# Kernel optimization log

Hardware: AMD Instinct MI355X
Metric: run time of the kernel (lower is better)

The kernel has to match this reference:

```python
import jax, jax.numpy as jnp
import numpy as np

LATENT_PACKET_SIZE = 16

def setup_inputs() -> dict:
    key = jax.random.key(0)
    z = jax.random.normal(key, (4096, 1, 8192), dtype=jnp.float32)
    return {"z": z}

def reference(z) -> jnp.ndarray:
    B = z.shape[0]
    D = z.shape[2]
    P = LATENT_PACKET_SIZE
    n_packets = D // P
    zp = z.reshape(B, n_packets, P)                      # (B, N, P)
    # sort packets within each sample by the first element of each packet
    inds = jnp.argsort(zp[:, :, 0], axis=1)              # (B, N) int
    z_ordered = jnp.take_along_axis(zp, inds[:, :, None], axis=1)  # batched gather
    return z_ordered.reshape(B, 1, n_packets * P)
```

## Files before the change

kernel.cpp:

```cpp
#include <hip/hip_runtime.h>


#define NPK 512
#define DIM 8192
#define RPB 4
#define NT  256

__global__ __launch_bounds__(NT, 8)
void sort_latent_kernel(const float* __restrict__ z, float* __restrict__ out) {
    __shared__ unsigned long long keys[RPB][NPK];
    __shared__ unsigned short     srcp[RPB][NPK];

    const int lane = threadIdx.x & 63;
    const int w    = threadIdx.x >> 6;
    const int row  = blockIdx.x * RPB + w;
    const float* __restrict__ rowin  = z   + (size_t)row * DIM;
    float*       __restrict__ rowout = out + (size_t)row * DIM;

    unsigned long long myk[8];
#pragma unroll
    for (int i = 0; i < 8; ++i) {
        const unsigned int p = (unsigned)(i * 64 + lane);
        const unsigned int b = __float_as_uint(rowin[p * 16]);
        const unsigned int u = b ^ (((unsigned)((int)b >> 31)) | 0x80000000u);
        myk[i] = ((unsigned long long)u << 32) | p;
        keys[w][p] = myk[i];
    }
    __syncthreads();

    unsigned int rank[8] = {0, 0, 0, 0, 0, 0, 0, 0};
    const unsigned long long* __restrict__ kk = keys[w];
    for (int j = 0; j < NPK; j += 2) {
        const unsigned long long k0 = kk[j];
        const unsigned long long k1 = kk[j + 1];
#pragma unroll
        for (int i = 0; i < 8; ++i) {
            rank[i] += (unsigned)(k0 < myk[i]);
            rank[i] += (unsigned)(k1 < myk[i]);
        }
    }
#pragma unroll
    for (int i = 0; i < 8; ++i)
        srcp[w][rank[i]] = (unsigned short)(i * 64 + lane);
    __syncthreads();

    const float4* __restrict__ in4  = (const float4*)rowin;
    float4*       __restrict__ out4 = (float4*)rowout;
#pragma unroll 8
    for (int i = 0; i < DIM / 4 / 64; ++i) {
        const int o = i * 64 + lane;
        const int s = (int)srcp[w][o >> 2];
        out4[o] = in4[(s << 2) | (o & 3)];
    }
}

extern "C" void kernel_launch(void* const* d_in, const int* in_sizes, int n_in,
                              void* d_out, int out_size, void* d_ws, size_t ws_size,
                              hipStream_t stream) {
    const float* z = (const float*)d_in[0];
    float* out = (float*)d_out;
    const int nrows = in_sizes[0] / DIM;
    sort_latent_kernel<<<nrows / RPB, NT, 0, stream>>>(z, out);
}
```

Before: 251.9 us.

## Replace O(N^2) rank counting with register bitonic sort using wave shuffles

Swaps the per-row all-pairs rank counting, which reads every key from LDS for each of 512 keys, for a bitonic sort. Each lane holds 8 consecutive keys in registers; small strides use in-register compare-exchange and larger strides use 64-bit cross-lane shuffles. This drops the keys LDS array and one barrier and cuts comparisons from about 256K to about 12K per row. The cost is many 64-bit shuffles, which need two DPP/permute ops each, and index-dependent select logic.

```diff
diff --git a/kernel.cpp b/kernel.cpp
--- a/kernel.cpp
+++ b/kernel.cpp
@@ -6,10 +6,18 @@
 #define RPB 4
 #define NT  256
 
+typedef unsigned long long u64;
+
+#define CEX(a, b, up) {                      \
+    bool sw = ((a) > (b)) == (up);           \
+    u64 t0 = sw ? (b) : (a);                 \
+    (b) = sw ? (a) : (b);                    \
+    (a) = t0;                                \
+}
+
 __global__ __launch_bounds__(NT, 8)
 void sort_latent_kernel(const float* __restrict__ z, float* __restrict__ out) {
-    __shared__ unsigned long long keys[RPB][NPK];
-    __shared__ unsigned short     srcp[RPB][NPK];
+    __shared__ unsigned short srcp[RPB][NPK];
 
     const int lane = threadIdx.x & 63;
     const int w    = threadIdx.x >> 6;
@@ -17,31 +25,46 @@
     const float* __restrict__ rowin  = z   + (size_t)row * DIM;
     float*       __restrict__ rowout = out + (size_t)row * DIM;
 
-    unsigned long long myk[8];
+    u64 v[8];
 #pragma unroll
-    for (int i = 0; i < 8; ++i) {
-        const unsigned int p = (unsigned)(i * 64 + lane);
-        const unsigned int b = __float_as_uint(rowin[p * 16]);
-        const unsigned int u = b ^ (((unsigned)((int)b >> 31)) | 0x80000000u);
-        myk[i] = ((unsigned long long)u << 32) | p;
-        keys[w][p] = myk[i];
+    for (int r = 0; r < 8; ++r) {
+        const unsigned p = (unsigned)(lane * 8 + r);
+        const unsigned b = __float_as_uint(rowin[p * 16]);
+        const unsigned u = b ^ (((unsigned)((int)b >> 31)) | 0x80000000u);
+        v[r] = ((u64)u << 32) | p;
     }
-    __syncthreads();
 
-    unsigned int rank[8] = {0, 0, 0, 0, 0, 0, 0, 0};
-    const unsigned long long* __restrict__ kk = keys[w];
-    for (int j = 0; j < NPK; j += 2) {
-        const unsigned long long k0 = kk[j];
-        const unsigned long long k1 = kk[j + 1];
+    CEX(v[0], v[1], true);  CEX(v[2], v[3], false);
+    CEX(v[4], v[5], true);  CEX(v[6], v[7], false);
+    CEX(v[0], v[2], true);  CEX(v[1], v[3], true);
+    CEX(v[4], v[6], false); CEX(v[5], v[7], false);
+    CEX(v[0], v[1], true);  CEX(v[2], v[3], true);
+    CEX(v[4], v[5], false); CEX(v[6], v[7], false);
+
+    for (int k = 8; k <= NPK; k <<= 1) {
+        const bool up = ((lane & (k >> 3)) == 0);
+        for (int j = k >> 1; j >= 8; j >>= 1) {
+            const int d = j >> 3;
+            const bool keepmin = (((lane & d) == 0) == up);
 #pragma unroll
-        for (int i = 0; i < 8; ++i) {
-            rank[i] += (unsigned)(k0 < myk[i]);
-            rank[i] += (unsigned)(k1 < myk[i]);
+            for (int r = 0; r < 8; ++r) {
+                const u64 o = __shfl_xor(v[r], d, 64);
+                const u64 mn = (v[r] < o) ? v[r] : o;
+                const u64 mx = v[r] ^ o ^ mn;
+                v[r] = keepmin ? mn : mx;
+            }
         }
+        CEX(v[0], v[4], up); CEX(v[1], v[5], up);
+        CEX(v[2], v[6], up); CEX(v[3], v[7], up);
+        CEX(v[0], v[2], up); CEX(v[1], v[3], up);
+        CEX(v[4], v[6], up); CEX(v[5], v[7], up);
+        CEX(v[0], v[1], up); CEX(v[2], v[3], up);
+        CEX(v[4], v[5], up); CEX(v[6], v[7], up);
     }
+
 #pragma unroll
-    for (int i = 0; i < 8; ++i)
-        srcp[w][rank[i]] = (unsigned short)(i * 64 + lane);
+    for (int r = 0; r < 8; ++r)
+        srcp[w][lane * 8 + r] = (unsigned short)(v[r] & (NPK - 1));
     __syncthreads();
 
     const float4* __restrict__ in4  = (const float4*)rowin;
```

Result: no change. 250.9 us (-0.4%).
